# Kernel optimization log

Measured on AMD Instinct MI355X. Metric: run time of the kernel, lower is better.

The kernel has to match this reference:

```python
import jax, jax.numpy as jnp
import numpy as np

DIM = 20
N = 200000
E = 6400000
ITERATIONS = 3


def setup_inputs() -> dict:
    key = jax.random.key(0)
    ks = jax.random.split(key, 20)
    inp = {
        "h": jax.random.normal(ks[0], (N, DIM), dtype=jnp.float32),
        "node2depth": jax.random.randint(ks[1], (N,), 0, 5, dtype=jnp.int32),
        "edge_src": jax.random.randint(ks[2], (E,), 0, N, dtype=jnp.int32),
        "edge_dst": jax.random.randint(ks[3], (E,), 0, N, dtype=jnp.int32),
    }
    # Six DIM x DIM Linear layers (weight stored [out,in] like torch, plus bias)
    scale = 1.0 / np.sqrt(DIM)
    names = ["Wz", "Uz", "Wr", "Ur", "Wh", "Uh"]
    for j, nm in enumerate(names):
        inp[nm + "_w"] = jax.random.uniform(ks[4 + 2 * j], (DIM, DIM), jnp.float32, -scale, scale)
        inp[nm + "_b"] = jax.random.uniform(ks[5 + 2 * j], (DIM,), jnp.float32, -scale, scale)
    return inp


def _linear(x, w, b):
    return x @ w.T + b


def reference(h, Wz_w, Wz_b, Uz_w, Uz_b, Wr_w, Wr_b, Ur_w, Ur_b,
              Wh_w, Wh_b, Uh_w, Uh_b, node2depth, edge_src, edge_dst):
    active = None
    for i in range(ITERATIONS):
        # active set shrinks as i grows (depth + i <= ITERATIONS)
        active = (node2depth + i) <= ITERATIONS  # [N] bool
        af = active.astype(h.dtype)
        # x[u] = sum over neighbors v of h[v], counting only active src AND active dst
        msg = h[edge_src] * af[edge_src][:, None]          # [E, DIM]
        x = jax.ops.segment_sum(msg, edge_dst, num_segments=N)  # [N, DIM]
        x = x * af[:, None]
        z = jax.nn.sigmoid(_linear(x, Wz_w, Wz_b) + _linear(h, Uz_w, Uz_b))
        r = jax.nn.sigmoid(_linear(x, Wr_w, Wr_b) + _linear(h, Ur_w, Ur_b))
        h_cand = jnp.tanh(_linear(x, Wh_w, Wh_b) + _linear(r * h, Uh_w, Uh_b))
        h_new = z * h + (1.0 - z) * h_cand
        # inactive nodes are dropped from the dict in the original; since the
        # active set only shrinks, keeping their old h is equivalent
        h = jnp.where(active[:, None], h_new, h)
    # original returns only nodes active at the last iteration; zero out the rest
    return jnp.where(active[:, None], h, jnp.zeros_like(h))
```

## Files before the change

### kernel.cpp

```cpp
#include <hip/hip_runtime.h>

#define DIM    20
#define NN     200000
#define EE     6400000
#define ITERS  3
#define BLOCK  256

#define NODES_PER_FINE   64
#define NFINE            3125
#define NCOARSE          98
#define FINE_PER_COARSE  32

#define TILE1            2048
#define IPT1             8

#define TILE             4096
#define IPT              16

#define CAP1             67584
#define NT2P             17
#define CAP2             2304
#define PIPT             9

typedef unsigned int u32;

__global__ void init_cursors(int* __restrict__ coarse_cursor,
                             int* __restrict__ fine_cursor,
                             int* __restrict__ gcur) {
    int g = blockIdx.x * 256 + threadIdx.x;
    if (g < NCOARSE) coarse_cursor[g] = g * CAP1;
    if (g < NFINE)   fine_cursor[g]   = g * CAP2;
    if (g == 0) *gcur = 0;
}

__global__ __launch_bounds__(BLOCK) void ctab_build(const int* __restrict__ depth,
                                                    u32* __restrict__ CT) {
    int i = blockIdx.x * BLOCK + threadIdx.x;
    if (i >= NN / 8) return;
    int4 a = *(const int4*)(depth + i * 8);
    int4 b = *(const int4*)(depth + i * 8 + 4);
    u32 w = ((u32)a.x & 7u)        | (((u32)a.y & 7u) << 4)
          | (((u32)a.z & 7u) << 8) | (((u32)a.w & 7u) << 12)
          | (((u32)b.x & 7u) << 16)| (((u32)b.y & 7u) << 20)
          | (((u32)b.z & 7u) << 24)| (((u32)b.w & 7u) << 28);
    CT[i] = w;
}

__global__ __launch_bounds__(BLOCK) void p1_split(const int* __restrict__ esrc,
                                                  const int* __restrict__ edst,
                                                  int* __restrict__ coarse_cursor,
                                                  u32* __restrict__ buf1) {
    __shared__ u32 hist[NCOARSE];
    __shared__ u32 lbase[NCOARSE];
    __shared__ u32 gbase[NCOARSE];
    __shared__ u32 lout[TILE1];
    int tid = threadIdx.x;
    int start = blockIdx.x * TILE1;
    if (tid < NCOARSE) hist[tid] = 0;
    __syncthreads();

    int4 d4[2], s4[2];
    #pragma unroll
    for (int q = 0; q < 2; ++q) {
        int e4 = start + (q * BLOCK + tid) * 4;
        d4[q] = *(const int4*)(edst + e4);
        s4[q] = *(const int4*)(esrc + e4);
    }
    int dd[IPT1], ss[IPT1];
    dd[0]=d4[0].x; dd[1]=d4[0].y; dd[2]=d4[0].z; dd[3]=d4[0].w;
    dd[4]=d4[1].x; dd[5]=d4[1].y; dd[6]=d4[1].z; dd[7]=d4[1].w;
    ss[0]=s4[0].x; ss[1]=s4[0].y; ss[2]=s4[0].z; ss[3]=s4[0].w;
    ss[4]=s4[1].x; ss[5]=s4[1].y; ss[6]=s4[1].z; ss[7]=s4[1].w;

    u32 rank[IPT1];
    #pragma unroll
    for (int k = 0; k < IPT1; ++k)
        rank[k] = atomicAdd(&hist[(u32)dd[k] >> 11], 1u);
    __syncthreads();

    if (tid < 64) {
        u32 a = hist[tid];
        u32 b = (tid + 64 < NCOARSE) ? hist[tid + 64] : 0u;
        u32 ia = a, ib = b;
        #pragma unroll
        for (int off = 1; off < 64; off <<= 1) {
            u32 ta = (u32)__shfl_up((int)ia, off, 64);
            u32 tb = (u32)__shfl_up((int)ib, off, 64);
            if (tid >= off) { ia += ta; ib += tb; }
        }
        u32 totA = (u32)__shfl((int)ia, 63, 64);
        lbase[tid] = ia - a;
        if (tid + 64 < NCOARSE) lbase[tid + 64] = totA + ib - b;
    }
    __syncthreads();
    if (tid < NCOARSE) {
        u32 cq = hist[tid];
        gbase[tid] = cq ? (u32)atomicAdd((u32*)&coarse_cursor[tid], cq) : 0u;
    }
    #pragma unroll
    for (int k = 0; k < IPT1; ++k)
        lout[lbase[(u32)dd[k] >> 11] + rank[k]] = ((u32)dd[k] & 2047u) | ((u32)ss[k] << 11);
    __syncthreads();
    int wid = tid >> 6, lane = tid & 63;
    for (int b = wid; b < NCOARSE; b += 4) {
        u32 cq = hist[b], lb = lbase[b], gb = gbase[b];
        for (u32 i = lane; i < cq; i += 64)
            buf1[gb + i] = lout[lb + i];
    }
}

__global__ __launch_bounds__(BLOCK) void p2_split(const u32* __restrict__ buf1,
                                                  const int* __restrict__ coarse_cursor,
                                                  int* __restrict__ fine_cursor,
                                                  u32* __restrict__ buf2) {
    int bid = blockIdx.x;
    int c = bid / NT2P, t = bid - c * NT2P;
    int base  = c * CAP1;
    int end   = coarse_cursor[c];
    int start = base + t * TILE;
    if (start >= end) return;

    __shared__ u32 hist[FINE_PER_COARSE];
    __shared__ u32 lbase[FINE_PER_COARSE];
    __shared__ u32 gbase[FINE_PER_COARSE];
    __shared__ u32 lout[TILE];
    int tid = threadIdx.x;
    if (tid < FINE_PER_COARSE) hist[tid] = 0;
    __syncthreads();

    u32 w[IPT];
    #pragma unroll
    for (int q = 0; q < 4; ++q) {
        int i4 = start + (q * BLOCK + tid) * 4;
        if (i4 + 3 < end) {
            uint4 v = *(const uint4*)(buf1 + i4);
            w[q * 4 + 0] = v.x; w[q * 4 + 1] = v.y;
            w[q * 4 + 2] = v.z; w[q * 4 + 3] = v.w;
        } else {
            #pragma unroll
            for (int j = 0; j < 4; ++j) {
                int i = i4 + j;
                w[q * 4 + j] = (i < end) ? buf1[i] : 0xFFFFFFFFu;
            }
        }
    }
    u32 rank[IPT];
    #pragma unroll
    for (int k = 0; k < IPT; ++k)
        if (w[k] != 0xFFFFFFFFu)
            rank[k] = atomicAdd(&hist[(w[k] & 2047u) >> 6], 1u);
    __syncthreads();

    if (tid < 32) {
        u32 a = hist[tid], ia = a;
        #pragma unroll
        for (int off = 1; off < 32; off <<= 1) {
            u32 ta = (u32)__shfl_up((int)ia, off, 32);
            if (tid >= off) ia += ta;
        }
        lbase[tid] = ia - a;
        int f = c * FINE_PER_COARSE + tid;
        gbase[tid] = a ? (u32)atomicAdd((u32*)&fine_cursor[f], a) : 0u;
    }
    __syncthreads();
    #pragma unroll
    for (int k = 0; k < IPT; ++k)
        if (w[k] != 0xFFFFFFFFu)
            lout[lbase[(w[k] & 2047u) >> 6] + rank[k]] = (w[k] & 63u) | ((w[k] >> 11) << 6);
    __syncthreads();
    int wid = tid >> 6, lane = tid & 63;
    for (int b = wid; b < FINE_PER_COARSE; b += 4) {
        u32 cq = hist[b], lb = lbase[b], gb = gbase[b];
        for (u32 i = lane; i < cq; i += 64)
            buf2[gb + i] = lout[lb + i];
    }
}

__global__ __launch_bounds__(BLOCK) void pb_sort(const u32* __restrict__ buf2,
                                                 const int* __restrict__ fine_cursor,
                                                 const u32* __restrict__ CT,
                                                 int* __restrict__ gcur,
                                                 int* __restrict__ ptr,
                                                 u32* __restrict__ cnt3,
                                                 u32* __restrict__ ssrc) {
    __shared__ u32 hist[512];
    __shared__ u32 ebase[512];
    __shared__ u32 lout[CAP2];
    __shared__ u32 wsum[4];
    __shared__ int slo;
    int tid = threadIdx.x;
    int f = blockIdx.x;
    int base = f * CAP2;
    int end  = fine_cursor[f];
    int cnt  = end - base;
    hist[tid] = 0; hist[tid + 256] = 0;
    __syncthreads();

    u32 w[PIPT];
    #pragma unroll
    for (int q = 0; q < 2; ++q) {
        int i4 = base + (q * BLOCK + tid) * 4;
        if (i4 + 3 < end) {
            uint4 v = *(const uint4*)(buf2 + i4);
            w[q * 4 + 0] = v.x; w[q * 4 + 1] = v.y;
            w[q * 4 + 2] = v.z; w[q * 4 + 3] = v.w;
        } else {
            #pragma unroll
            for (int j = 0; j < 4; ++j) {
                int i = i4 + j;
                w[q * 4 + j] = (i < end) ? buf2[i] : 0xFFFFFFFFu;
            }
        }
    }
    {
        int i = base + 2 * BLOCK * 4 + tid;
        w[8] = (i < end) ? buf2[i] : 0xFFFFFFFFu;
    }
    u32 cls[PIPT];
    #pragma unroll
    for (int k = 0; k < PIPT; ++k) {
        u32 s = w[k] >> 6;
        if (s > (u32)(NN - 1)) s = (u32)(NN - 1);
        cls[k] = (CT[s >> 3] >> ((s & 7u) << 2)) & 7u;
    }
    u32 key[PIPT], rank[PIPT];
    #pragma unroll
    for (int k = 0; k < PIPT; ++k) {
        if (w[k] != 0xFFFFFFFFu) {
            key[k]  = (w[k] & 63u) * 8u + cls[k];
            rank[k] = atomicAdd(&hist[key[k]], 1u);
        }
    }
    if (tid == 0) slo = atomicAdd(gcur, cnt);
    __syncthreads();
    {
        u32 s0 = hist[2 * tid], s1 = hist[2 * tid + 1];
        u32 s = s0 + s1;
        int lane = tid & 63, wid = tid >> 6;
        u32 incl = s;
        #pragma unroll
        for (int off = 1; off < 64; off <<= 1) {
            u32 t = __shfl_up((int)incl, off, 64);
            if (lane >= off) incl += t;
        }
        if (lane == 63) wsum[wid] = incl;
        __syncthreads();
        u32 woff = 0;
        for (int w2 = 0; w2 < wid; ++w2) woff += wsum[w2];
        u32 excl = woff + incl - s;
        ebase[2 * tid]     = excl;
        ebase[2 * tid + 1] = excl + s0;
    }
    __syncthreads();
    int lo = slo;
    if (tid < NODES_PER_FINE) {
        u32 base0 = ebase[tid * 8];
        u32 cc1 = ebase[tid * 8 + 2] - base0;
        u32 cc2 = ebase[tid * 8 + 3] - base0;
        u32 cc3 = ebase[tid * 8 + 4] - base0;
        int u = f * NODES_PER_FINE + tid;
        ptr[u]  = lo + (int)base0;
        cnt3[u] = cc1 | (cc2 << 10) | (cc3 << 20);
    }
    #pragma unroll
    for (int k = 0; k < PIPT; ++k) {
        if (w[k] != 0xFFFFFFFFu) lout[ebase[key[k]] + rank[k]] = w[k] >> 6;
    }
    __syncthreads();
    for (int j = tid; j < cnt; j += BLOCK) ssrc[lo + j] = lout[j];
}

__device__ __forceinline__ u32 pack_bf16x2(float a, float b) {
    u32 ua = __float_as_uint(a);
    u32 ub = __float_as_uint(b);
    ua = (ua + 0x7FFFu + ((ua >> 16) & 1u)) >> 16;
    ub = (ub + 0x7FFFu + ((ub >> 16) & 1u)) & 0xFFFF0000u;
    return ua | ub;
}

__global__ __launch_bounds__(BLOCK) void hconv(const float* __restrict__ h,
                                               u32* __restrict__ hbA,
                                               u32* __restrict__ hbC,
                                               const int* __restrict__ depth) {
    int g = blockIdx.x * BLOCK + threadIdx.x;
    if (g >= NN * 8) return;
    int node = g >> 3, s = g & 7;
    if (depth[node] > ITERS) return;
    float2 f = *(const float2*)(h + (size_t)node * DIM + s * 2);
    hbA[(size_t)node * 8 + s] = pack_bf16x2(f.x, f.y);
    if (s < 2) {
        float2 fc = *(const float2*)(h + (size_t)node * DIM + 16 + s * 2);
        hbC[(size_t)node * 2 + s] = pack_bf16x2(fc.x, fc.y);
    }
}


__device__ __forceinline__ float bl(u32 w) { return __uint_as_float(w << 16); }
__device__ __forceinline__ float bh(u32 w) { return __uint_as_float(w & 0xFFFF0000u); }

__device__ __forceinline__ void acc_half(float* xa, float* xc, uint4 a, u32 c) {
    xa[0]+=bl(a.x); xa[1]+=bh(a.x);
    xa[2]+=bl(a.y); xa[3]+=bh(a.y);
    xa[4]+=bl(a.z); xa[5]+=bh(a.z);
    xa[6]+=bl(a.w); xa[7]+=bh(a.w);
    xc[0]+=bl(c);   xc[1]+=bh(c);
}

__global__ __launch_bounds__(BLOCK) void gather_x(
    const u32* __restrict__ hbA, const u32* __restrict__ hbC,
    const int* __restrict__ depth, const int* __restrict__ ptr,
    const u32* __restrict__ cnt3, const u32* __restrict__ ssrc,
    float* __restrict__ xg, int lim, int shift)
{
    int tid = threadIdx.x;
    int u = blockIdx.x * 32 + (tid >> 3);
    int j = tid & 7;
    int r = j >> 1;
    int q = j & 1;
    if (depth[u] > lim) return;
    int p = ptr[u];
    int d = (int)((cnt3[u] >> shift) & 1023u);

    float xa[8], xc[2];
    #pragma unroll
    for (int k = 0; k < 8; ++k) xa[k] = 0.0f;
    xc[0] = 0.0f; xc[1] = 0.0f;

    int e = r;
    for (; e + 12 < d; e += 16) {
        u32 p0 = ssrc[p + e];
        u32 p1 = ssrc[p + e + 4];
        u32 p2 = ssrc[p + e + 8];
        u32 p3 = ssrc[p + e + 12];
        uint4 a0 = *(const uint4*)(hbA + (size_t)p0 * 8 + q * 4);
        uint4 a1 = *(const uint4*)(hbA + (size_t)p1 * 8 + q * 4);
        uint4 a2 = *(const uint4*)(hbA + (size_t)p2 * 8 + q * 4);
        uint4 a3 = *(const uint4*)(hbA + (size_t)p3 * 8 + q * 4);
        u32 c0 = hbC[(size_t)p0 * 2 + q];
        u32 c1 = hbC[(size_t)p1 * 2 + q];
        u32 c2 = hbC[(size_t)p2 * 2 + q];
        u32 c3 = hbC[(size_t)p3 * 2 + q];
        acc_half(xa, xc, a0, c0);
        acc_half(xa, xc, a1, c1);
        acc_half(xa, xc, a2, c2);
        acc_half(xa, xc, a3, c3);
    }
    for (; e + 4 < d; e += 8) {
        u32 p0 = ssrc[p + e];
        u32 p1 = ssrc[p + e + 4];
        uint4 a0 = *(const uint4*)(hbA + (size_t)p0 * 8 + q * 4);
        uint4 a1 = *(const uint4*)(hbA + (size_t)p1 * 8 + q * 4);
        u32 c0 = hbC[(size_t)p0 * 2 + q];
        u32 c1 = hbC[(size_t)p1 * 2 + q];
        acc_half(xa, xc, a0, c0);
        acc_half(xa, xc, a1, c1);
    }
    if (e < d) {
        u32 p0 = ssrc[p + e];
        uint4 a0 = *(const uint4*)(hbA + (size_t)p0 * 8 + q * 4);
        u32 c0 = hbC[(size_t)p0 * 2 + q];
        acc_half(xa, xc, a0, c0);
    }
    #pragma unroll
    for (int k = 0; k < 8; ++k) {
        xa[k] += __shfl_xor(xa[k], 2, 64);
        xa[k] += __shfl_xor(xa[k], 4, 64);
    }
    xc[0] += __shfl_xor(xc[0], 2, 64); xc[0] += __shfl_xor(xc[0], 4, 64);
    xc[1] += __shfl_xor(xc[1], 2, 64); xc[1] += __shfl_xor(xc[1], 4, 64);

    float* xr = xg + (size_t)u * DIM;
    if (j == 0) {
        *(float4*)(xr)      = make_float4(xa[0], xa[1], xa[2], xa[3]);
        *(float4*)(xr + 4)  = make_float4(xa[4], xa[5], xa[6], xa[7]);
        *(float2*)(xr + 16) = make_float2(xc[0], xc[1]);
    } else if (j == 1) {
        *(float4*)(xr + 8)  = make_float4(xa[0], xa[1], xa[2], xa[3]);
        *(float4*)(xr + 12) = make_float4(xa[4], xa[5], xa[6], xa[7]);
        *(float2*)(xr + 18) = make_float2(xc[0], xc[1]);
    }
}


__device__ __forceinline__ float fast_sigmoid(float t) {
    return 1.0f / (1.0f + __expf(-t));
}
__device__ __forceinline__ float fast_tanh(float t) {
    t = fminf(fmaxf(t, -15.0f), 15.0f);
    float e2 = __expf(2.0f * t);
    return (e2 - 1.0f) / (e2 + 1.0f);
}

__global__ __launch_bounds__(BLOCK) void gru_update(
    const float* __restrict__ xg,
    const float* __restrict__ h_in, float* __restrict__ h_out,
    u32* __restrict__ hbA, u32* __restrict__ hbC,
    const int* __restrict__ depth,
    const float* __restrict__ Wz, const float* __restrict__ bWz,
    const float* __restrict__ Uz, const float* __restrict__ bUz,
    const float* __restrict__ Wr, const float* __restrict__ bWr,
    const float* __restrict__ Ur, const float* __restrict__ bUr,
    const float* __restrict__ Wh, const float* __restrict__ bWh,
    const float* __restrict__ Uh, const float* __restrict__ bUh,
    int lim, int limNext, int isFinal)
{
    int u = blockIdx.x * BLOCK + threadIdx.x;
    if (u >= NN) return;
    int du = depth[u];
    bool act = du <= lim;
    if (!act) {
        if (isFinal) {
            float4 z4 = make_float4(0.f, 0.f, 0.f, 0.f);
            float4* o4 = (float4*)(h_out + (size_t)u * DIM);
            #pragma unroll
            for (int q = 0; q < 5; ++q) o4[q] = z4;
        }
        return;
    }

    float x[DIM], h[DIM];
    {
        const float4* xv = (const float4*)(xg + (size_t)u * DIM);
        float4 a0 = xv[0], a1 = xv[1], a2 = xv[2], a3 = xv[3], a4 = xv[4];
        x[0]=a0.x; x[1]=a0.y; x[2]=a0.z; x[3]=a0.w;
        x[4]=a1.x; x[5]=a1.y; x[6]=a1.z; x[7]=a1.w;
        x[8]=a2.x; x[9]=a2.y; x[10]=a2.z; x[11]=a2.w;
        x[12]=a3.x; x[13]=a3.y; x[14]=a3.z; x[15]=a3.w;
        x[16]=a4.x; x[17]=a4.y; x[18]=a4.z; x[19]=a4.w;
    }
    {
        const float4* hv = (const float4*)(h_in + (size_t)u * DIM);
        float4 a0 = hv[0], a1 = hv[1], a2 = hv[2], a3 = hv[3], a4 = hv[4];
        h[0]=a0.x; h[1]=a0.y; h[2]=a0.z; h[3]=a0.w;
        h[4]=a1.x; h[5]=a1.y; h[6]=a1.z; h[7]=a1.w;
        h[8]=a2.x; h[9]=a2.y; h[10]=a2.z; h[11]=a2.w;
        h[12]=a3.x; h[13]=a3.y; h[14]=a3.z; h[15]=a3.w;
        h[16]=a4.x; h[17]=a4.y; h[18]=a4.z; h[19]=a4.w;
    }

    float z[DIM], rh[DIM];
    #pragma unroll
    for (int j = 0; j < DIM; ++j) {
        float sz = bWz[j] + bUz[j];
        float sr = bWr[j] + bUr[j];
        #pragma unroll
        for (int k = 0; k < DIM; ++k) {
            sz += x[k] * Wz[j * DIM + k];
            sz += h[k] * Uz[j * DIM + k];
            sr += x[k] * Wr[j * DIM + k];
            sr += h[k] * Ur[j * DIM + k];
        }
        z[j]  = fast_sigmoid(sz);
        rh[j] = fast_sigmoid(sr) * h[j];
    }

    float o[DIM];
    #pragma unroll
    for (int j = 0; j < DIM; ++j) {
        float sh = bWh[j] + bUh[j];
        #pragma unroll
        for (int k = 0; k < DIM; ++k) {
            sh += x[k]  * Wh[j * DIM + k];
            sh += rh[k] * Uh[j * DIM + k];
        }
        float hc = fast_tanh(sh);
        o[j] = z[j] * h[j] + (1.0f - z[j]) * hc;
    }

    {
        float4* o4 = (float4*)(h_out + (size_t)u * DIM);
        o4[0] = make_float4(o[0],  o[1],  o[2],  o[3]);
        o4[1] = make_float4(o[4],  o[5],  o[6],  o[7]);
        o4[2] = make_float4(o[8],  o[9],  o[10], o[11]);
        o4[3] = make_float4(o[12], o[13], o[14], o[15]);
        o4[4] = make_float4(o[16], o[17], o[18], o[19]);
    }
    if (!isFinal && du <= limNext) {
        u32* rowA = hbA + (size_t)u * 8;
        uint4 wA0 = make_uint4(pack_bf16x2(o[0], o[1]),   pack_bf16x2(o[2], o[3]),
                               pack_bf16x2(o[4], o[5]),   pack_bf16x2(o[6], o[7]));
        uint4 wA1 = make_uint4(pack_bf16x2(o[8], o[9]),   pack_bf16x2(o[10], o[11]),
                               pack_bf16x2(o[12], o[13]), pack_bf16x2(o[14], o[15]));
        *(uint4*)rowA       = wA0;
        *(uint4*)(rowA + 4) = wA1;
        *(uint2*)(hbC + (size_t)u * 2) =
            make_uint2(pack_bf16x2(o[16], o[17]), pack_bf16x2(o[18], o[19]));
    }
}


extern "C" void kernel_launch(void* const* d_in, const int* in_sizes, int n_in,
                              void* d_out, int out_size, void* d_ws, size_t ws_size,
                              hipStream_t stream) {
    const float* h0    = (const float*)d_in[0];
    const int*   depth = (const int*)d_in[1];
    const int*   esrc  = (const int*)d_in[2];
    const int*   edst  = (const int*)d_in[3];
    const float* Wz  = (const float*)d_in[4];  const float* bWz = (const float*)d_in[5];
    const float* Uz  = (const float*)d_in[6];  const float* bUz = (const float*)d_in[7];
    const float* Wr  = (const float*)d_in[8];  const float* bWr = (const float*)d_in[9];
    const float* Ur  = (const float*)d_in[10]; const float* bUr = (const float*)d_in[11];
    const float* Wh  = (const float*)d_in[12]; const float* bWh = (const float*)d_in[13];
    const float* Uh  = (const float*)d_in[14]; const float* bUh = (const float*)d_in[15];
    float* out = (float*)d_out;

    int* W = (int*)d_ws;
    u32*  CT            = (u32*)(W + 0);
    int*  gcur          = W + 25024;
    int*  coarse_cursor = W + 25088;
    int*  fine_cursor   = W + 25216;
    int*  ptr           = W + 28416;
    u32*  cnt3          = (u32*)(W + 228416);
    u32*  buf1          = (u32*)(W + 428416);
    u32*  buf2          = buf1 + (size_t)NCOARSE * CAP1;
    float* h1           = (float*)(buf2 + (size_t)NFINE * CAP2);
    u32*  hbA           = (u32*)(h1 + (size_t)NN * DIM);
    u32*  hbC           = hbA + (size_t)NN * 8;
    u32*  ssrc          = buf1;
    float* xg           = (float*)buf2;

    init_cursors<<<13, 256, 0, stream>>>(coarse_cursor, fine_cursor, gcur);
    ctab_build  <<<(NN / 8 + BLOCK - 1) / BLOCK, BLOCK, 0, stream>>>(depth, CT);
    p1_split    <<<EE / TILE1, BLOCK, 0, stream>>>(esrc, edst, coarse_cursor, buf1);
    p2_split    <<<NCOARSE * NT2P, BLOCK, 0, stream>>>(buf1, coarse_cursor, fine_cursor, buf2);
    pb_sort     <<<NFINE, BLOCK, 0, stream>>>(buf2, fine_cursor, CT, gcur, ptr, cnt3, ssrc);
    hconv       <<<(NN * 8) / BLOCK, BLOCK, 0, stream>>>(h0, hbA, hbC, depth);

    gather_x  <<<NN / 32, BLOCK, 0, stream>>>(hbA, hbC, depth, ptr, cnt3, ssrc, xg, 3, 20);
    gru_update<<<(NN + BLOCK - 1) / BLOCK, BLOCK, 0, stream>>>(xg, h0, h1, hbA, hbC, depth,
        Wz, bWz, Uz, bUz, Wr, bWr, Ur, bUr, Wh, bWh, Uh, bUh, 3, 2, 0);
    gather_x  <<<NN / 32, BLOCK, 0, stream>>>(hbA, hbC, depth, ptr, cnt3, ssrc, xg, 2, 10);
    gru_update<<<(NN + BLOCK - 1) / BLOCK, BLOCK, 0, stream>>>(xg, h1, h1, hbA, hbC, depth,
        Wz, bWz, Uz, bUz, Wr, bWr, Ur, bUr, Wh, bWh, Uh, bUh, 2, 1, 0);
    gather_x  <<<NN / 32, BLOCK, 0, stream>>>(hbA, hbC, depth, ptr, cnt3, ssrc, xg, 1, 0);
    gru_update<<<(NN + BLOCK - 1) / BLOCK, BLOCK, 0, stream>>>(xg, h1, out, hbA, hbC, depth,
        Wz, bWz, Uz, bUz, Wr, bWr, Ur, bUr, Wh, bWh, Uh, bUh, 1, 0, 1);
}
```

Before: 530.3 us.

## Fuse neighbor gather into GRU update kernel and merge setup kernels

The per-iteration gather and GRU update are merged into one kernel. Gathered x sums are staged in shared memory instead of being written to a global buffer and read back. The bf16 neighbor-feature buffers become ping-pong, so one iteration's reads do not race with its writes. The cursor init, depth table build and bf16 conversion kernels are merged into one setup kernel to cut launches. In exchange, only a quarter of each block's threads run the GRU math after the barrier, and extra workspace is needed for the second bf16 buffer.

```diff
diff --git a/kernel.cpp b/kernel.cpp
--- a/kernel.cpp
+++ b/kernel.cpp
@@ -22,28 +22,46 @@
 #define CAP2             2304
 #define PIPT             9
 
+#define XSTRIDE          21
+
 typedef unsigned int u32;
 
-__global__ void init_cursors(int* __restrict__ coarse_cursor,
-                             int* __restrict__ fine_cursor,
-                             int* __restrict__ gcur) {
-    int g = blockIdx.x * 256 + threadIdx.x;
+__device__ __forceinline__ u32 pack_bf16x2(float a, float b) {
+    u32 ua = __float_as_uint(a);
+    u32 ub = __float_as_uint(b);
+    ua = (ua + 0x7FFFu + ((ua >> 16) & 1u)) >> 16;
+    ub = (ub + 0x7FFFu + ((ub >> 16) & 1u)) & 0xFFFF0000u;
+    return ua | ub;
+}
+
+__global__ __launch_bounds__(BLOCK) void setup(const float* __restrict__ h,
+                                               const int* __restrict__ depth,
+                                               u32* __restrict__ hbA,
+                                               u32* __restrict__ hbC,
+                                               u32* __restrict__ CT,
+                                               int* __restrict__ coarse_cursor,
+                                               int* __restrict__ fine_cursor,
+                                               int* __restrict__ gcur) {
+    int g = blockIdx.x * BLOCK + threadIdx.x;
     if (g < NCOARSE) coarse_cursor[g] = g * CAP1;
     if (g < NFINE)   fine_cursor[g]   = g * CAP2;
     if (g == 0) *gcur = 0;
-}
-
-__global__ __launch_bounds__(BLOCK) void ctab_build(const int* __restrict__ depth,
-                                                    u32* __restrict__ CT) {
-    int i = blockIdx.x * BLOCK + threadIdx.x;
-    if (i >= NN / 8) return;
-    int4 a = *(const int4*)(depth + i * 8);
-    int4 b = *(const int4*)(depth + i * 8 + 4);
-    u32 w = ((u32)a.x & 7u)        | (((u32)a.y & 7u) << 4)
-          | (((u32)a.z & 7u) << 8) | (((u32)a.w & 7u) << 12)
-          | (((u32)b.x & 7u) << 16)| (((u32)b.y & 7u) << 20)
-          | (((u32)b.z & 7u) << 24)| (((u32)b.w & 7u) << 28);
-    CT[i] = w;
+    if (g < NN / 8) {
+        int4 a = *(const int4*)(depth + g * 8);
+        int4 b = *(const int4*)(depth + g * 8 + 4);
+        CT[g] = ((u32)a.x & 7u)        | (((u32)a.y & 7u) << 4)
+              | (((u32)a.z & 7u) << 8) | (((u32)a.w & 7u) << 12)
+              | (((u32)b.x & 7u) << 16)| (((u32)b.y & 7u) << 20)
+              | (((u32)b.z & 7u) << 24)| (((u32)b.w & 7u) << 28);
+    }
+    int node = g >> 3, s = g & 7;
+    if (depth[node] > ITERS) return;
+    float2 f = *(const float2*)(h + (size_t)node * DIM + s * 2);
+    hbA[(size_t)node * 8 + s] = pack_bf16x2(f.x, f.y);
+    if (s < 2) {
+        float2 fc = *(const float2*)(h + (size_t)node * DIM + 16 + s * 2);
+        hbC[(size_t)node * 2 + s] = pack_bf16x2(fc.x, fc.y);
+    }
 }
 
 __global__ __launch_bounds__(BLOCK) void p1_split(const int* __restrict__ esrc,
@@ -270,30 +288,6 @@
     for (int j = tid; j < cnt; j += BLOCK) ssrc[lo + j] = lout[j];
 }
 
-__device__ __forceinline__ u32 pack_bf16x2(float a, float b) {
-    u32 ua = __float_as_uint(a);
-    u32 ub = __float_as_uint(b);
-    ua = (ua + 0x7FFFu + ((ua >> 16) & 1u)) >> 16;
-    ub = (ub + 0x7FFFu + ((ub >> 16) & 1u)) & 0xFFFF0000u;
-    return ua | ub;
-}
-
-__global__ __launch_bounds__(BLOCK) void hconv(const float* __restrict__ h,
-                                               u32* __restrict__ hbA,
-                                               u32* __restrict__ hbC,
-                                               const int* __restrict__ depth) {
-    int g = blockIdx.x * BLOCK + threadIdx.x;
-    if (g >= NN * 8) return;
-    int node = g >> 3, s = g & 7;
-    if (depth[node] > ITERS) return;
-    float2 f = *(const float2*)(h + (size_t)node * DIM + s * 2);
-    hbA[(size_t)node * 8 + s] = pack_bf16x2(f.x, f.y);
-    if (s < 2) {
-        float2 fc = *(const float2*)(h + (size_t)node * DIM + 16 + s * 2);
-        hbC[(size_t)node * 2 + s] = pack_bf16x2(fc.x, fc.y);
-    }
-}
-
 
 __device__ __forceinline__ float bl(u32 w) { return __uint_as_float(w << 16); }
 __device__ __forceinline__ float bh(u32 w) { return __uint_as_float(w & 0xFFFF0000u); }
@@ -306,82 +300,6 @@
     xc[0]+=bl(c);   xc[1]+=bh(c);
 }
 
-__global__ __launch_bounds__(BLOCK) void gather_x(
-    const u32* __restrict__ hbA, const u32* __restrict__ hbC,
-    const int* __restrict__ depth, const int* __restrict__ ptr,
-    const u32* __restrict__ cnt3, const u32* __restrict__ ssrc,
-    float* __restrict__ xg, int lim, int shift)
-{
-    int tid = threadIdx.x;
-    int u = blockIdx.x * 32 + (tid >> 3);
-    int j = tid & 7;
-    int r = j >> 1;
-    int q = j & 1;
-    if (depth[u] > lim) return;
-    int p = ptr[u];
-    int d = (int)((cnt3[u] >> shift) & 1023u);
-
-    float xa[8], xc[2];
-    #pragma unroll
-    for (int k = 0; k < 8; ++k) xa[k] = 0.0f;
-    xc[0] = 0.0f; xc[1] = 0.0f;
-
-    int e = r;
-    for (; e + 12 < d; e += 16) {
-        u32 p0 = ssrc[p + e];
-        u32 p1 = ssrc[p + e + 4];
-        u32 p2 = ssrc[p + e + 8];
-        u32 p3 = ssrc[p + e + 12];
-        uint4 a0 = *(const uint4*)(hbA + (size_t)p0 * 8 + q * 4);
-        uint4 a1 = *(const uint4*)(hbA + (size_t)p1 * 8 + q * 4);
-        uint4 a2 = *(const uint4*)(hbA + (size_t)p2 * 8 + q * 4);
-        uint4 a3 = *(const uint4*)(hbA + (size_t)p3 * 8 + q * 4);
-        u32 c0 = hbC[(size_t)p0 * 2 + q];
-        u32 c1 = hbC[(size_t)p1 * 2 + q];
-        u32 c2 = hbC[(size_t)p2 * 2 + q];
-        u32 c3 = hbC[(size_t)p3 * 2 + q];
-        acc_half(xa, xc, a0, c0);
-        acc_half(xa, xc, a1, c1);
-        acc_half(xa, xc, a2, c2);
-        acc_half(xa, xc, a3, c3);
-    }
-    for (; e + 4 < d; e += 8) {
-        u32 p0 = ssrc[p + e];
-        u32 p1 = ssrc[p + e + 4];
-        uint4 a0 = *(const uint4*)(hbA + (size_t)p0 * 8 + q * 4);
-        uint4 a1 = *(const uint4*)(hbA + (size_t)p1 * 8 + q * 4);
-        u32 c0 = hbC[(size_t)p0 * 2 + q];
-        u32 c1 = hbC[(size_t)p1 * 2 + q];
-        acc_half(xa, xc, a0, c0);
-        acc_half(xa, xc, a1, c1);
-    }
-    if (e < d) {
-        u32 p0 = ssrc[p + e];
-        uint4 a0 = *(const uint4*)(hbA + (size_t)p0 * 8 + q * 4);
-        u32 c0 = hbC[(size_t)p0 * 2 + q];
-        acc_half(xa, xc, a0, c0);
-    }
-    #pragma unroll
-    for (int k = 0; k < 8; ++k) {
-        xa[k] += __shfl_xor(xa[k], 2, 64);
-        xa[k] += __shfl_xor(xa[k], 4, 64);
-    }
-    xc[0] += __shfl_xor(xc[0], 2, 64); xc[0] += __shfl_xor(xc[0], 4, 64);
-    xc[1] += __shfl_xor(xc[1], 2, 64); xc[1] += __shfl_xor(xc[1], 4, 64);
-
-    float* xr = xg + (size_t)u * DIM;
-    if (j == 0) {
-        *(float4*)(xr)      = make_float4(xa[0], xa[1], xa[2], xa[3]);
-        *(float4*)(xr + 4)  = make_float4(xa[4], xa[5], xa[6], xa[7]);
-        *(float2*)(xr + 16) = make_float2(xc[0], xc[1]);
-    } else if (j == 1) {
-        *(float4*)(xr + 8)  = make_float4(xa[0], xa[1], xa[2], xa[3]);
-        *(float4*)(xr + 12) = make_float4(xa[4], xa[5], xa[6], xa[7]);
-        *(float2*)(xr + 18) = make_float2(xc[0], xc[1]);
-    }
-}
-
-
 __device__ __forceinline__ float fast_sigmoid(float t) {
     return 1.0f / (1.0f + __expf(-t));
 }
@@ -391,43 +309,111 @@
     return (e2 - 1.0f) / (e2 + 1.0f);
 }
 
-__global__ __launch_bounds__(BLOCK) void gru_update(
-    const float* __restrict__ xg,
+__global__ __launch_bounds__(BLOCK) void grnn_iter(
+    const u32* __restrict__ hbA_in, const u32* __restrict__ hbC_in,
+    u32* __restrict__ hbA_out, u32* __restrict__ hbC_out,
     const float* __restrict__ h_in, float* __restrict__ h_out,
-    u32* __restrict__ hbA, u32* __restrict__ hbC,
-    const int* __restrict__ depth,
+    const int* __restrict__ depth, const int* __restrict__ ptr,
+    const u32* __restrict__ cnt3, const u32* __restrict__ ssrc,
     const float* __restrict__ Wz, const float* __restrict__ bWz,
     const float* __restrict__ Uz, const float* __restrict__ bUz,
     const float* __restrict__ Wr, const float* __restrict__ bWr,
     const float* __restrict__ Ur, const float* __restrict__ bUr,
     const float* __restrict__ Wh, const float* __restrict__ bWh,
     const float* __restrict__ Uh, const float* __restrict__ bUh,
-    int lim, int limNext, int isFinal)
+    int lim, int limNext, int shift, int isFinal)
 {
-    int u = blockIdx.x * BLOCK + threadIdx.x;
-    if (u >= NN) return;
+    __shared__ float xl[64 * XSTRIDE];
+    int tid = threadIdx.x;
+    int t = tid & 7, team = tid >> 3;
+    int r = t >> 1, q = t & 1;
+
+    #pragma unroll
+    for (int rep = 0; rep < 2; ++rep) {
+        int nl = team + rep * 32;
+        int u = blockIdx.x * 64 + nl;
+        if (depth[u] <= lim) {
+            int p = ptr[u];
+            int d = (int)((cnt3[u] >> shift) & 1023u);
+
+            float xa[8], xc[2];
+            #pragma unroll
+            for (int k = 0; k < 8; ++k) xa[k] = 0.0f;
+            xc[0] = 0.0f; xc[1] = 0.0f;
+
+            int e = r;
+            for (; e + 12 < d; e += 16) {
+                u32 p0 = ssrc[p + e];
+                u32 p1 = ssrc[p + e + 4];
+                u32 p2 = ssrc[p + e + 8];
+                u32 p3 = ssrc[p + e + 12];
+                uint4 a0 = *(const uint4*)(hbA_in + (size_t)p0 * 8 + q * 4);
+                uint4 a1 = *(const uint4*)(hbA_in + (size_t)p1 * 8 + q * 4);
+                uint4 a2 = *(const uint4*)(hbA_in + (size_t)p2 * 8 + q * 4);
+                uint4 a3 = *(const uint4*)(hbA_in + (size_t)p3 * 8 + q * 4);
+                u32 c0 = hbC_in[(size_t)p0 * 2 + q];
+                u32 c1 = hbC_in[(size_t)p1 * 2 + q];
+                u32 c2 = hbC_in[(size_t)p2 * 2 + q];
+                u32 c3 = hbC_in[(size_t)p3 * 2 + q];
+                acc_half(xa, xc, a0, c0);
+                acc_half(xa, xc, a1, c1);
+                acc_half(xa, xc, a2, c2);
+                acc_half(xa, xc, a3, c3);
+            }
+            for (; e + 4 < d; e += 8) {
+                u32 p0 = ssrc[p + e];
+                u32 p1 = ssrc[p + e + 4];
+                uint4 a0 = *(const uint4*)(hbA_in + (size_t)p0 * 8 + q * 4);
+                uint4 a1 = *(const uint4*)(hbA_in + (size_t)p1 * 8 + q * 4);
+                u32 c0 = hbC_in[(size_t)p0 * 2 + q];
+                u32 c1 = hbC_in[(size_t)p1 * 2 + q];
+                acc_half(xa, xc, a0, c0);
+                acc_half(xa, xc, a1, c1);
+            }
+            if (e < d) {
+                u32 p0 = ssrc[p + e];
+                uint4 a0 = *(const uint4*)(hbA_in + (size_t)p0 * 8 + q * 4);
+                u32 c0 = hbC_in[(size_t)p0 * 2 + q];
+                acc_half(xa, xc, a0, c0);
+            }
+            #pragma unroll
+            for (int k = 0; k < 8; ++k) {
+                xa[k] += __shfl_xor(xa[k], 2, 64);
+                xa[k] += __shfl_xor(xa[k], 4, 64);
+            }
+            xc[0] += __shfl_xor(xc[0], 2, 64); xc[0] += __shfl_xor(xc[0], 4, 64);
+            xc[1] += __shfl_xor(xc[1], 2, 64); xc[1] += __shfl_xor(xc[1], 4, 64);
+
+            float* xr = xl + nl * XSTRIDE;
+            if (t == 0) {
+                #pragma unroll
+                for (int k = 0; k < 8; ++k) xr[k] = xa[k];
+                xr[16] = xc[0]; xr[17] = xc[1];
+            } else if (t == 1) {
+                #pragma unroll
+                for (int k = 0; k < 8; ++k) xr[8 + k] = xa[k];
+                xr[18] = xc[0]; xr[19] = xc[1];
+            }
+        }
+    }
+    __syncthreads();
+    if (tid >= 64) return;
+
+    int u = blockIdx.x * 64 + tid;
     int du = depth[u];
-    bool act = du <= lim;
-    if (!act) {
+    if (du > lim) {
         if (isFinal) {
             float4 z4 = make_float4(0.f, 0.f, 0.f, 0.f);
             float4* o4 = (float4*)(h_out + (size_t)u * DIM);
             #pragma unroll
-            for (int q = 0; q < 5; ++q) o4[q] = z4;
+            for (int qq = 0; qq < 5; ++qq) o4[qq] = z4;
         }
         return;
     }
 
     float x[DIM], h[DIM];
-    {
-        const float4* xv = (const float4*)(xg + (size_t)u * DIM);
-        float4 a0 = xv[0], a1 = xv[1], a2 = xv[2], a3 = xv[3], a4 = xv[4];
-        x[0]=a0.x; x[1]=a0.y; x[2]=a0.z; x[3]=a0.w;
-        x[4]=a1.x; x[5]=a1.y; x[6]=a1.z; x[7]=a1.w;
-        x[8]=a2.x; x[9]=a2.y; x[10]=a2.z; x[11]=a2.w;
-        x[12]=a3.x; x[13]=a3.y; x[14]=a3.z; x[15]=a3.w;
-        x[16]=a4.x; x[17]=a4.y; x[18]=a4.z; x[19]=a4.w;
-    }
+    #pragma unroll
+    for (int k = 0; k < DIM; ++k) x[k] = xl[tid * XSTRIDE + k];
     {
         const float4* hv = (const float4*)(h_in + (size_t)u * DIM);
         float4 a0 = hv[0], a1 = hv[1], a2 = hv[2], a3 = hv[3], a4 = hv[4];
@@ -476,14 +462,14 @@
         o4[4] = make_float4(o[16], o[17], o[18], o[19]);
     }
     if (!isFinal && du <= limNext) {
-        u32* rowA = hbA + (size_t)u * 8;
+        u32* rowA = hbA_out + (size_t)u * 8;
         uint4 wA0 = make_uint4(pack_bf16x2(o[0], o[1]),   pack_bf16x2(o[2], o[3]),
                                pack_bf16x2(o[4], o[5]),   pack_bf16x2(o[6], o[7]));
         uint4 wA1 = make_uint4(pack_bf16x2(o[8], o[9]),   pack_bf16x2(o[10], o[11]),
                                pack_bf16x2(o[12], o[13]), pack_bf16x2(o[14], o[15]));
         *(uint4*)rowA       = wA0;
         *(uint4*)(rowA + 4) = wA1;
-        *(uint2*)(hbC + (size_t)u * 2) =
+        *(uint2*)(hbC_out + (size_t)u * 2) =
             make_uint2(pack_bf16x2(o[16], o[17]), pack_bf16x2(o[18], o[19]));
     }
 }
@@ -514,25 +500,25 @@
     u32*  buf1          = (u32*)(W + 428416);
     u32*  buf2          = buf1 + (size_t)NCOARSE * CAP1;
     float* h1           = (float*)(buf2 + (size_t)NFINE * CAP2);
-    u32*  hbA           = (u32*)(h1 + (size_t)NN * DIM);
-    u32*  hbC           = hbA + (size_t)NN * 8;
+    u32*  hbA0          = (u32*)(h1 + (size_t)NN * DIM);
+    u32*  hbC0          = hbA0 + (size_t)NN * 8;
+    u32*  hbA1          = hbC0 + (size_t)NN * 2;
+    u32*  hbC1          = hbA1 + (size_t)NN * 8;
     u32*  ssrc          = buf1;
-    float* xg           = (float*)buf2;
-
-    init_cursors<<<13, 256, 0, stream>>>(coarse_cursor, fine_cursor, gcur);
-    ctab_build  <<<(NN / 8 + BLOCK - 1) / BLOCK, BLOCK, 0, stream>>>(depth, CT);
-    p1_split    <<<EE / TILE1, BLOCK, 0, stream>>>(esrc, edst, coarse_cursor, buf1);
-    p2_split    <<<NCOARSE * NT2P, BLOCK, 0, stream>>>(buf1, coarse_cursor, fine_cursor, buf2);
-    pb_sort     <<<NFINE, BLOCK, 0, stream>>>(buf2, fine_cursor, CT, gcur, ptr, cnt3, ssrc);
-    hconv       <<<(NN * 8) / BLOCK, BLOCK, 0, stream>>>(h0, hbA, hbC, depth);
-
-    gather_x  <<<NN / 32, BLOCK, 0, stream>>>(hbA, hbC, depth, ptr, cnt3, ssrc, xg, 3, 20);
-    gru_update<<<(NN + BLOCK - 1) / BLOCK, BLOCK, 0, stream>>>(xg, h0, h1, hbA, hbC, depth,
-        Wz, bWz, Uz, bUz, Wr, bWr, Ur, bUr, Wh, bWh, Uh, bUh, 3, 2, 0);
-    gather_x  <<<NN / 32, BLOCK, 0, stream>>>(hbA, hbC, depth, ptr, cnt3, ssrc, xg, 2, 10);
-    gru_update<<<(NN + BLOCK - 1) / BLOCK, BLOCK, 0, stream>>>(xg, h1, h1, hbA, hbC, depth,
-        Wz, bWz, Uz, bUz, Wr, bWr, Ur, bUr, Wh, bWh, Uh, bUh, 2, 1, 0);
-    gather_x  <<<NN / 32, BLOCK, 0, stream>>>(hbA, hbC, depth, ptr, cnt3, ssrc, xg, 1, 0);
-    gru_update<<<(NN + BLOCK - 1) / BLOCK, BLOCK, 0, stream>>>(xg, h1, out, hbA, hbC, depth,
-        Wz, bWz, Uz, bUz, Wr, bWr, Ur, bUr, Wh, bWh, Uh, bUh, 1, 0, 1);
-}
+
+    setup   <<<(NN * 8) / BLOCK, BLOCK, 0, stream>>>(h0, depth, hbA0, hbC0, CT,
+                                                     coarse_cursor, fine_cursor, gcur);
+    p1_split<<<EE / TILE1, BLOCK, 0, stream>>>(esrc, edst, coarse_cursor, buf1);
+    p2_split<<<NCOARSE * NT2P, BLOCK, 0, stream>>>(buf1, coarse_cursor, fine_cursor, buf2);
+    pb_sort <<<NFINE, BLOCK, 0, stream>>>(buf2, fine_cursor, CT, gcur, ptr, cnt3, ssrc);
+
+    grnn_iter<<<NN / 64, BLOCK, 0, stream>>>(hbA0, hbC0, hbA1, hbC1, h0, h1,
+        depth, ptr, cnt3, ssrc,
+        Wz, bWz, Uz, bUz, Wr, bWr, Ur, bUr, Wh, bWh, Uh, bUh, 3, 2, 20, 0);
+    grnn_iter<<<NN / 64, BLOCK, 0, stream>>>(hbA1, hbC1, hbA0, hbC0, h1, h1,
+        depth, ptr, cnt3, ssrc,
+        Wz, bWz, Uz, bUz, Wr, bWr, Ur, bUr, Wh, bWh, Uh, bUh, 2, 1, 10, 0);
+    grnn_iter<<<NN / 64, BLOCK, 0, stream>>>(hbA0, hbC0, hbA1, hbC1, h1, out,
+        depth, ptr, cnt3, ssrc,
+        Wz, bWz, Uz, bUz, Wr, bWr, Ur, bUr, Wh, bWh, Uh, bUh, 1, 0, 0, 1);
+}
```

After: 507.1 us. 1.05x faster.
